# Optimization experiments

Measured on AMD Instinct MI355X. Metric: run time of the kernel, lower is better.

Reference implementation:

```python
import jax, jax.numpy as jnp
import numpy as np

GROUPS = 8
EPS = 1e-5


def setup_inputs() -> dict:
    key = jax.random.key(0)
    ks = jax.random.split(key, 4)
    B, C, H, W = 8, 128, 128, 128
    s = 1.0 / np.sqrt(C)
    return {
        "x": jax.random.normal(ks[0], (B, C, H, W), dtype=jnp.float32),
        "Wq": jax.random.normal(ks[1], (C, C), dtype=jnp.float32) * s,
        "bq": jnp.zeros((C,), jnp.float32),
        "Wk": jax.random.normal(ks[2], (C, C), dtype=jnp.float32) * s,
        "bk": jnp.zeros((C,), jnp.float32),
        "Wv": jax.random.normal(ks[3], (C, C), dtype=jnp.float32) * s,
        "bv": jnp.zeros((C,), jnp.float32),
        "gn_weight": jnp.ones((C,), jnp.float32),
        "gn_bias": jnp.zeros((C,), jnp.float32),
    }


def _group_norm(x_bcs, weight, bias):
    # x_bcs: [B, C, S]; GroupNorm over (C//G, S) per group
    B, C, S = x_bcs.shape
    xg = x_bcs.reshape(B, GROUPS, C // GROUPS, S)
    mean = xg.mean(axis=(2, 3), keepdims=True)
    var = jnp.mean(jnp.square(xg - mean), axis=(2, 3), keepdims=True)
    xn = ((xg - mean) * jax.lax.rsqrt(var + EPS)).reshape(B, C, S)
    return xn * weight[None, :, None] + bias[None, :, None]


def reference(x, Wq, bq, Wk, bk, Wv, bv, gn_weight, gn_bias):
    B, C, H, W = x.shape
    xs = x.reshape(B, C, H * W).transpose(0, 2, 1)  # [B, S, C]
    Q = xs @ Wq.T + bq
    K = xs @ Wk.T + bk
    V = xs @ Wv.T + bv
    Q = jax.nn.softmax(Q, axis=1)  # softmax over seq dim
    K = jax.nn.softmax(K, axis=1)
    KV = jnp.einsum('bsc,bsd->bcd', K, V)   # [B, C, C]
    Z = jnp.einsum('bsc,bcd->bsd', Q, KV)   # [B, S, C]
    xs = xs + Z
    x_gn = _group_norm(xs.transpose(0, 2, 1), gn_weight, gn_bias)  # [B, C, S]
    # Faithful to original: permute to [B, S, C] then view as [B, C, H, W]
    out = x_gn.transpose(0, 2, 1).reshape(B, C, H, W)
    return out
```

## Files before the change

kernel.cpp:

```cpp
#include <hip/hip_runtime.h>


#define Bn 8
#define Cn 128
#define Sn 16384
#define Gn 8

typedef float f32x4 __attribute__((ext_vector_type(4)));
typedef __bf16 bf16x8 __attribute__((ext_vector_type(8)));
typedef __bf16 bf16x4 __attribute__((ext_vector_type(4)));
typedef unsigned short u16;

__device__ __forceinline__ u16 f2bf(float f) {
    __bf16 h = (__bf16)f;
    return __builtin_bit_cast(u16, h);
}

__global__ __launch_bounds__(256) void k_wconv(const float* __restrict__ Wq,
                                               const float* __restrict__ Wk,
                                               const float* __restrict__ Wv,
                                               u16* __restrict__ Wb) {
    int i = blockIdx.x * 256 + threadIdx.x;
    const float* src = (i < 16384) ? Wq : (i < 32768 ? Wk : Wv);
    int j = i & 16383;
    Wb[i] = f2bf(src[j]);
}

__global__ __launch_bounds__(256) void k_tr(const float* __restrict__ x, u16* __restrict__ XT) {
    __shared__ float t[64][65];
    const int b = blockIdx.z, c0 = blockIdx.y * 64, s0 = blockIdx.x * 64;
    const int tid = threadIdx.x;
    const float* xb = x + ((size_t)b * Cn + c0) * Sn + s0;
#pragma unroll
    for (int i = 0; i < 16; ++i) {
        int n = tid + i * 256;
        int cl = n >> 6, sl = n & 63;
        t[cl][sl] = xb[(size_t)cl * Sn + sl];
    }
    __syncthreads();
    u16* xtb = XT + ((size_t)b * Sn + s0) * Cn + c0;
#pragma unroll
    for (int i = 0; i < 16; ++i) {
        int n = tid + i * 256;
        int sl = n >> 6, cl = n & 63;
        xtb[(size_t)sl * Cn + cl] = f2bf(t[cl][sl]);
    }
}

__device__ __forceinline__ bf16x8 lds_frag128(const u16* lds, int row, int c_off) {
    int ch = c_off >> 3;
    return *(const bf16x8*)(&lds[row * Cn + ((ch ^ (row & 7)) << 3)]);
}

__global__ __launch_bounds__(256) void k_qkv(
    const u16* __restrict__ XT, const u16* __restrict__ Wb,
    const float* __restrict__ bq, const float* __restrict__ bk, const float* __restrict__ bv,
    u16* __restrict__ EQ, u16* __restrict__ EK, u16* __restrict__ Vt,
    float* __restrict__ Zq, float* __restrict__ Zk) {
    __shared__ __align__(16) u16 tile[128 * 128];
    const int b = blockIdx.y;
    const int s0 = blockIdx.x * 128;
    const int tid = threadIdx.x;
    const int w = tid >> 6, l = tid & 63;
    const int l15 = l & 15, lq = l >> 4;

    {
        const u16* g = XT + ((size_t)b * Sn + s0) * Cn;
#pragma unroll
        for (int i = 0; i < 8; ++i) {
            int n = tid + i * 256, row = n >> 4, ch = n & 15;
            bf16x8 v = *(const bf16x8*)(g + row * Cn + ch * 8);
            *(bf16x8*)(&tile[row * Cn + ((ch ^ (row & 7)) << 3)]) = v;
        }
    }
    __syncthreads();

    const u16* Wqb = Wb;
    const u16* Wkb = Wb + 16384;
    const u16* Wvb = Wb + 32768;

    {
        bf16x8 a[2][4];
#pragma unroll
        for (int m = 0; m < 2; ++m)
#pragma unroll
            for (int k = 0; k < 4; ++k) {
                int row = 32 * w + 16 * m + l15;
                a[m][k] = *(const bf16x8*)(Wqb + row * Cn + 32 * k + lq * 8);
            }
        f32x4 acc[2][8];
#pragma unroll
        for (int m = 0; m < 2; ++m)
#pragma unroll
            for (int n = 0; n < 8; ++n)
#pragma unroll
                for (int r = 0; r < 4; ++r) acc[m][n][r] = 0.f;
#pragma unroll
        for (int n = 0; n < 8; ++n)
#pragma unroll
            for (int k = 0; k < 4; ++k) {
                bf16x8 bf = lds_frag128(tile, 16 * n + l15, 32 * k + lq * 8);
                acc[0][n] = __builtin_amdgcn_mfma_f32_16x16x32_bf16(a[0][k], bf, acc[0][n], 0, 0, 0);
                acc[1][n] = __builtin_amdgcn_mfma_f32_16x16x32_bf16(a[1][k], bf, acc[1][n], 0, 0, 0);
            }
        float zq[2][4] = {};
        float bqv[2][4];
#pragma unroll
        for (int m = 0; m < 2; ++m)
#pragma unroll
            for (int r = 0; r < 4; ++r) bqv[m][r] = bq[32 * w + 16 * m + lq * 4 + r];
#pragma unroll
        for (int m = 0; m < 2; ++m) {
            int cp = 32 * w + 16 * m + lq * 4;
#pragma unroll
            for (int n = 0; n < 8; ++n) {
                int s = s0 + 16 * n + l15;
                bf16x4 pk;
#pragma unroll
                for (int r = 0; r < 4; ++r) {
                    float e = __expf(acc[m][n][r] + bqv[m][r]);
                    zq[m][r] += e;
                    pk[r] = (__bf16)e;
                }
                *(bf16x4*)(&EQ[((size_t)b * Sn + s) * Cn + cp]) = pk;
            }
        }
#pragma unroll
        for (int m = 0; m < 2; ++m)
#pragma unroll
            for (int r = 0; r < 4; ++r) {
                float v = zq[m][r];
                v += __shfl_xor(v, 1);
                v += __shfl_xor(v, 2);
                v += __shfl_xor(v, 4);
                v += __shfl_xor(v, 8);
                if (l15 == 0) atomicAdd(&Zq[b * Cn + 32 * w + 16 * m + lq * 4 + r], v);
            }
    }

    bf16x8 am[2][4];
#pragma unroll
    for (int m = 0; m < 2; ++m)
#pragma unroll
        for (int k = 0; k < 4; ++k)
            am[m][k] = lds_frag128(tile, 32 * w + 16 * m + l15, 32 * k + lq * 8);

#pragma unroll
    for (int pass = 0; pass < 2; ++pass) {
        const u16* Wp = pass ? Wvb : Wkb;
        const float* bp = pass ? bv : bk;
        u16* Op = pass ? Vt : EK;
        f32x4 acc[2][8];
#pragma unroll
        for (int m = 0; m < 2; ++m)
#pragma unroll
            for (int n = 0; n < 8; ++n)
#pragma unroll
                for (int r = 0; r < 4; ++r) acc[m][n][r] = 0.f;
        float bval[8];
#pragma unroll
        for (int n = 0; n < 8; ++n) bval[n] = bp[16 * n + l15];
#pragma unroll
        for (int n = 0; n < 8; ++n)
#pragma unroll
            for (int k = 0; k < 4; ++k) {
                bf16x8 bf = *(const bf16x8*)(Wp + (16 * n + l15) * Cn + 32 * k + lq * 8);
                acc[0][n] = __builtin_amdgcn_mfma_f32_16x16x32_bf16(am[0][k], bf, acc[0][n], 0, 0, 0);
                acc[1][n] = __builtin_amdgcn_mfma_f32_16x16x32_bf16(am[1][k], bf, acc[1][n], 0, 0, 0);
            }
        float zk[8] = {};
#pragma unroll
        for (int m = 0; m < 2; ++m) {
            int sb = s0 + 32 * w + 16 * m + lq * 4;
#pragma unroll
            for (int n = 0; n < 8; ++n) {
                int cp = 16 * n + l15;
                bf16x4 pk;
#pragma unroll
                for (int r = 0; r < 4; ++r) {
                    float e = acc[m][n][r] + bval[n];
                    if (pass == 0) {
                        e = __expf(e);
                        zk[n] += e;
                    }
                    pk[r] = (__bf16)e;
                }
                *(bf16x4*)(&Op[((size_t)b * Cn + cp) * Sn + sb]) = pk;
            }
        }
        if (pass == 0) {
#pragma unroll
            for (int n = 0; n < 8; ++n) {
                float v = zk[n];
                v += __shfl_xor(v, 16);
                v += __shfl_xor(v, 32);
                if (l < 16) atomicAdd(&Zk[b * Cn + 16 * n + l], v);
            }
        }
    }
}

__global__ __launch_bounds__(512) void k_kv(const u16* __restrict__ EK, const u16* __restrict__ Vt,
                                            float* __restrict__ KVu) {
    __shared__ __align__(16) u16 ekt[128 * 64];
    __shared__ __align__(16) u16 vtt[128 * 64];
    const int b = blockIdx.y, sw = blockIdx.x;
    const int tid = threadIdx.x, w = tid >> 6, l = tid & 63;
    const int l15 = l & 15, lq = l >> 4;
    f32x4 acc[8];
#pragma unroll
    for (int n = 0; n < 8; ++n)
#pragma unroll
        for (int r = 0; r < 4; ++r) acc[n][r] = 0.f;
    const u16* ekb = EK + (size_t)b * Cn * Sn;
    const u16* vtb = Vt + (size_t)b * Cn * Sn;
    for (int step = 0; step < 8; ++step) {
        int s0 = sw * 512 + step * 64;
        __syncthreads();
#pragma unroll
        for (int i = 0; i < 2; ++i) {
            int n = tid + i * 512, row = n >> 3, ch = n & 7;
            int lidx = row * 64 + ((ch ^ (row & 7)) << 3);
            *(bf16x8*)(&ekt[lidx]) = *(const bf16x8*)(ekb + (size_t)row * Sn + s0 + ch * 8);
            *(bf16x8*)(&vtt[lidx]) = *(const bf16x8*)(vtb + (size_t)row * Sn + s0 + ch * 8);
        }
        __syncthreads();
#pragma unroll
        for (int k = 0; k < 2; ++k) {
            int ach = 4 * k + lq;
            int arow = 16 * w + l15;
            bf16x8 af = *(const bf16x8*)(&ekt[arow * 64 + ((ach ^ (arow & 7)) << 3)]);
#pragma unroll
            for (int n = 0; n < 8; ++n) {
                int brow = 16 * n + l15;
                bf16x8 bf = *(const bf16x8*)(&vtt[brow * 64 + ((ach ^ (brow & 7)) << 3)]);
                acc[n] = __builtin_amdgcn_mfma_f32_16x16x32_bf16(af, bf, acc[n], 0, 0, 0);
            }
        }
    }
#pragma unroll
    for (int n = 0; n < 8; ++n)
#pragma unroll
        for (int r = 0; r < 4; ++r) {
            int c = 16 * w + lq * 4 + r, d = 16 * n + l15;
            atomicAdd(&KVu[((size_t)b * Cn + c) * Cn + d], acc[n][r]);
        }
}

__global__ __launch_bounds__(256) void k_kvnorm(const float* __restrict__ KVu,
                                                const float* __restrict__ Zq,
                                                const float* __restrict__ Zk,
                                                u16* __restrict__ KV2T) {
    __shared__ float zi[128];
    __shared__ u16 t[128 * 136];
    const int b = blockIdx.x, tid = threadIdx.x;
    if (tid < 128) zi[tid] = 1.f / (Zk[b * Cn + tid] * Zq[b * Cn + tid]);
    __syncthreads();
    for (int i = 0; i < 64; ++i) {
        int n = tid + i * 256, c = n >> 7, d = n & 127;
        t[c * 136 + d] = f2bf(KVu[((size_t)b * Cn + c) * Cn + d] * zi[c]);
    }
    __syncthreads();
    for (int i = 0; i < 64; ++i) {
        int n = tid + i * 256, d = n >> 7, c = n & 127;
        KV2T[((size_t)b * Cn + d) * Cn + c] = t[c * 136 + d];
    }
}

__global__ __launch_bounds__(256) void k_z(
    const u16* __restrict__ EQ, const u16* __restrict__ KV2T, const u16* __restrict__ XT,
    u16* __restrict__ ybuf, float* __restrict__ gsum, float* __restrict__ gsq) {
    __shared__ __align__(16) u16 tile[128 * 128];
    const int b = blockIdx.y, s0 = blockIdx.x * 128;
    const int tid = threadIdx.x, w = tid >> 6, l = tid & 63;
    const int l15 = l & 15, lq = l >> 4;
    {
        const u16* g = EQ + ((size_t)b * Sn + s0) * Cn;
#pragma unroll
        for (int i = 0; i < 8; ++i) {
            int n = tid + i * 256, row = n >> 4, ch = n & 15;
            bf16x8 v = *(const bf16x8*)(g + row * Cn + ch * 8);
            *(bf16x8*)(&tile[row * Cn + ((ch ^ (row & 7)) << 3)]) = v;
        }
    }
    __syncthreads();
    bf16x8 a[2][4];
#pragma unroll
    for (int m = 0; m < 2; ++m)
#pragma unroll
        for (int k = 0; k < 4; ++k) {
            int rd = 32 * w + 16 * m + l15;
            a[m][k] = *(const bf16x8*)(KV2T + ((size_t)b * Cn + rd) * Cn + 32 * k + lq * 8);
        }
    f32x4 acc[2][8];
#pragma unroll
    for (int m = 0; m < 2; ++m)
#pragma unroll
        for (int n = 0; n < 8; ++n)
#pragma unroll
            for (int r = 0; r < 4; ++r) acc[m][n][r] = 0.f;
#pragma unroll
    for (int n = 0; n < 8; ++n)
#pragma unroll
        for (int k = 0; k < 4; ++k) {
            bf16x8 bf = lds_frag128(tile, 16 * n + l15, 32 * k + lq * 8);
            acc[0][n] = __builtin_amdgcn_mfma_f32_16x16x32_bf16(a[0][k], bf, acc[0][n], 0, 0, 0);
            acc[1][n] = __builtin_amdgcn_mfma_f32_16x16x32_bf16(a[1][k], bf, acc[1][n], 0, 0, 0);
        }
    float sm[2] = {0.f, 0.f}, sq[2] = {0.f, 0.f};
#pragma unroll
    for (int m = 0; m < 2; ++m) {
        int db = 32 * w + 16 * m + lq * 4;
#pragma unroll
        for (int n = 0; n < 8; ++n) {
            int s = s0 + 16 * n + l15;
            bf16x4 xv = *(const bf16x4*)(XT + ((size_t)b * Sn + s) * Cn + db);
            bf16x4 yk;
#pragma unroll
            for (int r = 0; r < 4; ++r) {
                float yv = (float)xv[r] + acc[m][n][r];
                sm[m] += yv;
                sq[m] += yv * yv;
                yk[r] = (__bf16)yv;
            }
            *(bf16x4*)(&ybuf[((size_t)b * Sn + s) * Cn + db]) = yk;
        }
    }
#pragma unroll
    for (int m = 0; m < 2; ++m) {
        float v1 = sm[m], v2 = sq[m];
#pragma unroll
        for (int mask = 1; mask < 64; mask <<= 1) {
            v1 += __shfl_xor(v1, mask);
            v2 += __shfl_xor(v2, mask);
        }
        if (l == 0) {
            int g = 2 * w + m;
            atomicAdd(&gsum[b * Gn + g], v1);
            atomicAdd(&gsq[b * Gn + g], v2);
        }
    }
}

__global__ __launch_bounds__(256) void k_gn(const u16* __restrict__ ybuf,
                                            const float* __restrict__ gsum,
                                            const float* __restrict__ gsq,
                                            const float* __restrict__ gnw,
                                            const float* __restrict__ gnb,
                                            float* __restrict__ out) {
    const float invN = 1.f / (float)(16 * Sn);
    size_t idx = (size_t)blockIdx.x * 256 + threadIdx.x;
    const size_t total = (size_t)Bn * Sn * Cn / 8;
    for (; idx < total; idx += (size_t)gridDim.x * 256) {
        size_t e0 = idx * 8;
        int c0 = (int)(e0 & 127);
        int b = (int)(e0 >> 21);
        int g = c0 >> 4;
        float mean = gsum[b * Gn + g] * invN;
        float var = gsq[b * Gn + g] * invN - mean * mean;
        float rstd = rsqrtf(var + 1e-5f);
        bf16x8 yv = *(const bf16x8*)(ybuf + e0);
        f32x4 o0, o1;
#pragma unroll
        for (int r = 0; r < 4; ++r) o0[r] = ((float)yv[r] - mean) * rstd * gnw[c0 + r] + gnb[c0 + r];
#pragma unroll
        for (int r = 0; r < 4; ++r) o1[r] = ((float)yv[4 + r] - mean) * rstd * gnw[c0 + 4 + r] + gnb[c0 + 4 + r];
        *(f32x4*)(out + e0) = o0;
        *(f32x4*)(out + e0 + 4) = o1;
    }
}

static constexpr size_t XT_OFF = 0;
static constexpr size_t EQ_OFF = 33554432;
static constexpr size_t EK_OFF = 67108864;
static constexpr size_t VT_OFF = 100663296;
static constexpr size_t WB_OFF = 134217728;
static constexpr size_t KVU_OFF = WB_OFF + 98304;
static constexpr size_t ZQ_OFF = KVU_OFF + 524288;
static constexpr size_t ZK_OFF = ZQ_OFF + 4096;
static constexpr size_t GSUM_OFF = ZK_OFF + 4096;
static constexpr size_t GSQ_OFF = GSUM_OFF + 256;
static constexpr size_t KV2T_OFF = GSQ_OFF + 256;
static constexpr size_t MEMSET_BYTES = 524288 + 4096 + 4096 + 256 + 256;

extern "C" void kernel_launch(void* const* d_in, const int* in_sizes, int n_in,
                              void* d_out, int out_size, void* d_ws, size_t ws_size,
                              hipStream_t stream) {
    const float* x = (const float*)d_in[0];
    const float* Wq = (const float*)d_in[1];
    const float* bq = (const float*)d_in[2];
    const float* Wk = (const float*)d_in[3];
    const float* bk = (const float*)d_in[4];
    const float* Wv = (const float*)d_in[5];
    const float* bv = (const float*)d_in[6];
    const float* gnw = (const float*)d_in[7];
    const float* gnb = (const float*)d_in[8];
    float* out = (float*)d_out;
    char* ws = (char*)d_ws;

    u16* XT = (u16*)(ws + XT_OFF);
    u16* EQ = (u16*)(ws + EQ_OFF);
    u16* EK = (u16*)(ws + EK_OFF);
    u16* Vt = (u16*)(ws + VT_OFF);
    u16* Wb = (u16*)(ws + WB_OFF);
    float* KVu = (float*)(ws + KVU_OFF);
    float* Zq = (float*)(ws + ZQ_OFF);
    float* Zk = (float*)(ws + ZK_OFF);
    float* Gsum = (float*)(ws + GSUM_OFF);
    float* Gsq = (float*)(ws + GSQ_OFF);
    u16* KV2T = (u16*)(ws + KV2T_OFF);
    u16* Ybuf = EK;

    hipMemsetAsync(ws + KVU_OFF, 0, MEMSET_BYTES, stream);
    k_wconv<<<dim3(192), dim3(256), 0, stream>>>(Wq, Wk, Wv, Wb);
    k_tr<<<dim3(Sn / 64, Cn / 64, Bn), dim3(256), 0, stream>>>(x, XT);
    k_qkv<<<dim3(Sn / 128, Bn), dim3(256), 0, stream>>>(XT, Wb, bq, bk, bv, EQ, EK, Vt, Zq, Zk);
    k_kv<<<dim3(32, Bn), dim3(512), 0, stream>>>(EK, Vt, KVu);
    k_kvnorm<<<dim3(Bn), dim3(256), 0, stream>>>(KVu, Zq, Zk, KV2T);
    k_z<<<dim3(Sn / 128, Bn), dim3(256), 0, stream>>>(EQ, KV2T, XT, Ybuf, Gsum, Gsq);
    k_gn<<<dim3(8192), dim3(256), 0, stream>>>(Ybuf, Gsum, Gsq, gnw, gnb, out);
}
```

Baseline: 338.5 us.

## Halve seq tiles in qkv/z kernels, vectorize transpose, reduce Zk atomics via LDS

The transpose kernel now uses float4 global loads and 16-byte bf16x8 stores in place of scalar accesses. k_qkv and k_z process 64-row sequence tiles instead of 128, which doubles the grid and cuts LDS and register use per block. k_qkv also reduces the Zk partial sums across waves in shared memory before issuing one atomic per channel. k_kv uses fewer blocks, each covering a longer sequence range. Together these aim for better occupancy and memory efficiency, at the cost of reloading the weight fragments in more blocks and issuing more Zq atomics.

```diff
diff --git a/kernel.cpp b/kernel.cpp
--- a/kernel.cpp
+++ b/kernel.cpp
@@ -32,18 +32,23 @@
     const int tid = threadIdx.x;
     const float* xb = x + ((size_t)b * Cn + c0) * Sn + s0;
 #pragma unroll
-    for (int i = 0; i < 16; ++i) {
+    for (int i = 0; i < 4; ++i) {
         int n = tid + i * 256;
-        int cl = n >> 6, sl = n & 63;
-        t[cl][sl] = xb[(size_t)cl * Sn + sl];
+        int cl = n >> 4, s4 = (n & 15) * 4;
+        f32x4 v = *(const f32x4*)(xb + (size_t)cl * Sn + s4);
+#pragma unroll
+        for (int j = 0; j < 4; ++j) t[cl][s4 + j] = v[j];
     }
     __syncthreads();
     u16* xtb = XT + ((size_t)b * Sn + s0) * Cn + c0;
 #pragma unroll
-    for (int i = 0; i < 16; ++i) {
+    for (int i = 0; i < 2; ++i) {
         int n = tid + i * 256;
-        int sl = n >> 6, cl = n & 63;
-        xtb[(size_t)sl * Cn + cl] = f2bf(t[cl][sl]);
+        int sl = n >> 3, cl0 = (n & 7) * 8;
+        bf16x8 o;
+#pragma unroll
+        for (int j = 0; j < 8; ++j) o[j] = (__bf16)t[cl0 + j][sl];
+        *(bf16x8*)(xtb + sl * Cn + cl0) = o;
     }
 }
 
@@ -57,9 +62,10 @@
     const float* __restrict__ bq, const float* __restrict__ bk, const float* __restrict__ bv,
     u16* __restrict__ EQ, u16* __restrict__ EK, u16* __restrict__ Vt,
     float* __restrict__ Zq, float* __restrict__ Zk) {
-    __shared__ __align__(16) u16 tile[128 * 128];
+    __shared__ __align__(16) u16 tile[64 * 128];
+    __shared__ float zbuf[4 * 128];
     const int b = blockIdx.y;
-    const int s0 = blockIdx.x * 128;
+    const int s0 = blockIdx.x * 64;
     const int tid = threadIdx.x;
     const int w = tid >> 6, l = tid & 63;
     const int l15 = l & 15, lq = l >> 4;
@@ -67,7 +73,7 @@
     {
         const u16* g = XT + ((size_t)b * Sn + s0) * Cn;
 #pragma unroll
-        for (int i = 0; i < 8; ++i) {
+        for (int i = 0; i < 4; ++i) {
             int n = tid + i * 256, row = n >> 4, ch = n & 15;
             bf16x8 v = *(const bf16x8*)(g + row * Cn + ch * 8);
             *(bf16x8*)(&tile[row * Cn + ((ch ^ (row & 7)) << 3)]) = v;
@@ -88,15 +94,15 @@
                 int row = 32 * w + 16 * m + l15;
                 a[m][k] = *(const bf16x8*)(Wqb + row * Cn + 32 * k + lq * 8);
             }
-        f32x4 acc[2][8];
+        f32x4 acc[2][4];
 #pragma unroll
         for (int m = 0; m < 2; ++m)
 #pragma unroll
-            for (int n = 0; n < 8; ++n)
+            for (int n = 0; n < 4; ++n)
 #pragma unroll
                 for (int r = 0; r < 4; ++r) acc[m][n][r] = 0.f;
 #pragma unroll
-        for (int n = 0; n < 8; ++n)
+        for (int n = 0; n < 4; ++n)
 #pragma unroll
             for (int k = 0; k < 4; ++k) {
                 bf16x8 bf = lds_frag128(tile, 16 * n + l15, 32 * k + lq * 8);
@@ -113,7 +119,7 @@
         for (int m = 0; m < 2; ++m) {
             int cp = 32 * w + 16 * m + lq * 4;
 #pragma unroll
-            for (int n = 0; n < 8; ++n) {
+            for (int n = 0; n < 4; ++n) {
                 int s = s0 + 16 * n + l15;
                 bf16x4 pk;
 #pragma unroll
@@ -138,25 +144,21 @@
             }
     }
 
-    bf16x8 am[2][4];
-#pragma unroll
-    for (int m = 0; m < 2; ++m)
-#pragma unroll
-        for (int k = 0; k < 4; ++k)
-            am[m][k] = lds_frag128(tile, 32 * w + 16 * m + l15, 32 * k + lq * 8);
+    bf16x8 am[4];
+#pragma unroll
+    for (int k = 0; k < 4; ++k)
+        am[k] = lds_frag128(tile, 16 * w + l15, 32 * k + lq * 8);
 
 #pragma unroll
     for (int pass = 0; pass < 2; ++pass) {
         const u16* Wp = pass ? Wvb : Wkb;
         const float* bp = pass ? bv : bk;
         u16* Op = pass ? Vt : EK;
-        f32x4 acc[2][8];
-#pragma unroll
-        for (int m = 0; m < 2; ++m)
-#pragma unroll
-            for (int n = 0; n < 8; ++n)
-#pragma unroll
-                for (int r = 0; r < 4; ++r) acc[m][n][r] = 0.f;
+        f32x4 acc[8];
+#pragma unroll
+        for (int n = 0; n < 8; ++n)
+#pragma unroll
+            for (int r = 0; r < 4; ++r) acc[n][r] = 0.f;
         float bval[8];
 #pragma unroll
         for (int n = 0; n < 8; ++n) bval[n] = bp[16 * n + l15];
@@ -165,28 +167,24 @@
 #pragma unroll
             for (int k = 0; k < 4; ++k) {
                 bf16x8 bf = *(const bf16x8*)(Wp + (16 * n + l15) * Cn + 32 * k + lq * 8);
-                acc[0][n] = __builtin_amdgcn_mfma_f32_16x16x32_bf16(am[0][k], bf, acc[0][n], 0, 0, 0);
-                acc[1][n] = __builtin_amdgcn_mfma_f32_16x16x32_bf16(am[1][k], bf, acc[1][n], 0, 0, 0);
+                acc[n] = __builtin_amdgcn_mfma_f32_16x16x32_bf16(am[k], bf, acc[n], 0, 0, 0);
             }
         float zk[8] = {};
-#pragma unroll
-        for (int m = 0; m < 2; ++m) {
-            int sb = s0 + 32 * w + 16 * m + lq * 4;
-#pragma unroll
-            for (int n = 0; n < 8; ++n) {
-                int cp = 16 * n + l15;
-                bf16x4 pk;
-#pragma unroll
-                for (int r = 0; r < 4; ++r) {
-                    float e = acc[m][n][r] + bval[n];
-                    if (pass == 0) {
-                        e = __expf(e);
-                        zk[n] += e;
-                    }
-                    pk[r] = (__bf16)e;
+        int sb = s0 + 16 * w + lq * 4;
+#pragma unroll
+        for (int n = 0; n < 8; ++n) {
+            int cp = 16 * n + l15;
+            bf16x4 pk;
+#pragma unroll
+            for (int r = 0; r < 4; ++r) {
+                float e = acc[n][r] + bval[n];
+                if (pass == 0) {
+                    e = __expf(e);
+                    zk[n] += e;
                 }
-                *(bf16x4*)(&Op[((size_t)b * Cn + cp) * Sn + sb]) = pk;
-            }
+                pk[r] = (__bf16)e;
+            }
+            *(bf16x4*)(&Op[((size_t)b * Cn + cp) * Sn + sb]) = pk;
         }
         if (pass == 0) {
 #pragma unroll
@@ -194,9 +192,14 @@
                 float v = zk[n];
                 v += __shfl_xor(v, 16);
                 v += __shfl_xor(v, 32);
-                if (l < 16) atomicAdd(&Zk[b * Cn + 16 * n + l], v);
-            }
-        }
+                if (l < 16) zbuf[w * 128 + 16 * n + l] = v;
+            }
+        }
+    }
+    __syncthreads();
+    if (tid < 128) {
+        float v = zbuf[tid] + zbuf[128 + tid] + zbuf[256 + tid] + zbuf[384 + tid];
+        atomicAdd(&Zk[b * Cn + tid], v);
     }
 }
 
@@ -214,8 +217,8 @@
         for (int r = 0; r < 4; ++r) acc[n][r] = 0.f;
     const u16* ekb = EK + (size_t)b * Cn * Sn;
     const u16* vtb = Vt + (size_t)b * Cn * Sn;
-    for (int step = 0; step < 8; ++step) {
-        int s0 = sw * 512 + step * 64;
+    for (int step = 0; step < 16; ++step) {
+        int s0 = sw * 1024 + step * 64;
         __syncthreads();
 #pragma unroll
         for (int i = 0; i < 2; ++i) {
@@ -270,14 +273,14 @@
 __global__ __launch_bounds__(256) void k_z(
     const u16* __restrict__ EQ, const u16* __restrict__ KV2T, const u16* __restrict__ XT,
     u16* __restrict__ ybuf, float* __restrict__ gsum, float* __restrict__ gsq) {
-    __shared__ __align__(16) u16 tile[128 * 128];
-    const int b = blockIdx.y, s0 = blockIdx.x * 128;
+    __shared__ __align__(16) u16 tile[64 * 128];
+    const int b = blockIdx.y, s0 = blockIdx.x * 64;
     const int tid = threadIdx.x, w = tid >> 6, l = tid & 63;
     const int l15 = l & 15, lq = l >> 4;
     {
         const u16* g = EQ + ((size_t)b * Sn + s0) * Cn;
 #pragma unroll
-        for (int i = 0; i < 8; ++i) {
+        for (int i = 0; i < 4; ++i) {
             int n = tid + i * 256, row = n >> 4, ch = n & 15;
             bf16x8 v = *(const bf16x8*)(g + row * Cn + ch * 8);
             *(bf16x8*)(&tile[row * Cn + ((ch ^ (row & 7)) << 3)]) = v;
@@ -292,15 +295,15 @@
             int rd = 32 * w + 16 * m + l15;
             a[m][k] = *(const bf16x8*)(KV2T + ((size_t)b * Cn + rd) * Cn + 32 * k + lq * 8);
         }
-    f32x4 acc[2][8];
+    f32x4 acc[2][4];
 #pragma unroll
     for (int m = 0; m < 2; ++m)
 #pragma unroll
-        for (int n = 0; n < 8; ++n)
+        for (int n = 0; n < 4; ++n)
 #pragma unroll
             for (int r = 0; r < 4; ++r) acc[m][n][r] = 0.f;
 #pragma unroll
-    for (int n = 0; n < 8; ++n)
+    for (int n = 0; n < 4; ++n)
 #pragma unroll
         for (int k = 0; k < 4; ++k) {
             bf16x8 bf = lds_frag128(tile, 16 * n + l15, 32 * k + lq * 8);
@@ -312,7 +315,7 @@
     for (int m = 0; m < 2; ++m) {
         int db = 32 * w + 16 * m + lq * 4;
 #pragma unroll
-        for (int n = 0; n < 8; ++n) {
+        for (int n = 0; n < 4; ++n) {
             int s = s0 + 16 * n + l15;
             bf16x4 xv = *(const bf16x4*)(XT + ((size_t)b * Sn + s) * Cn + db);
             bf16x4 yk;
@@ -414,9 +417,9 @@
     hipMemsetAsync(ws + KVU_OFF, 0, MEMSET_BYTES, stream);
     k_wconv<<<dim3(192), dim3(256), 0, stream>>>(Wq, Wk, Wv, Wb);
     k_tr<<<dim3(Sn / 64, Cn / 64, Bn), dim3(256), 0, stream>>>(x, XT);
-    k_qkv<<<dim3(Sn / 128, Bn), dim3(256), 0, stream>>>(XT, Wb, bq, bk, bv, EQ, EK, Vt, Zq, Zk);
-    k_kv<<<dim3(32, Bn), dim3(512), 0, stream>>>(EK, Vt, KVu);
+    k_qkv<<<dim3(Sn / 64, Bn), dim3(256), 0, stream>>>(XT, Wb, bq, bk, bv, EQ, EK, Vt, Zq, Zk);
+    k_kv<<<dim3(16, Bn), dim3(512), 0, stream>>>(EK, Vt, KVu);
     k_kvnorm<<<dim3(Bn), dim3(256), 0, stream>>>(KVu, Zq, Zk, KV2T);
-    k_z<<<dim3(Sn / 128, Bn), dim3(256), 0, stream>>>(EQ, KV2T, XT, Ybuf, Gsum, Gsq);
+    k_z<<<dim3(Sn / 64, Bn), dim3(256), 0, stream>>>(EQ, KV2T, XT, Ybuf, Gsum, Gsq);
     k_gn<<<dim3(8192), dim3(256), 0, stream>>>(Ybuf, Gsum, Gsq, gnw, gnb, out);
 }
```

New measurement: 465.2 us. 1.37x slower.

## Stage kernel outputs through LDS for coalesced stores and vectorize transpose

Applied to the files above, without the earlier changes.

The transpose kernel now uses 16-byte float4 loads and 8-wide bf16 stores. The QKV kernel stages its EQ, EK and Vt outputs through swizzled shared memory so each is written as full coalesced rows, and it reduces the Zk partial sums per block before issuing atomics. The Z kernel processes two 128-row tiles per block, reads the residual XT through LDS, and writes ybuf through LDS with coalesced stores, which halves the grid and the number of atomics. These changes target scattered 8-byte global stores and strided loads, at the cost of extra barriers and LDS traffic.

```diff
diff --git a/kernel.cpp b/kernel.cpp
--- a/kernel.cpp
+++ b/kernel.cpp
@@ -32,24 +32,38 @@
     const int tid = threadIdx.x;
     const float* xb = x + ((size_t)b * Cn + c0) * Sn + s0;
 #pragma unroll
-    for (int i = 0; i < 16; ++i) {
+    for (int i = 0; i < 4; ++i) {
         int n = tid + i * 256;
-        int cl = n >> 6, sl = n & 63;
-        t[cl][sl] = xb[(size_t)cl * Sn + sl];
+        int cl = n >> 4, s4 = (n & 15) * 4;
+        f32x4 v = *(const f32x4*)(xb + (size_t)cl * Sn + s4);
+#pragma unroll
+        for (int j = 0; j < 4; ++j) t[cl][s4 + j] = v[j];
     }
     __syncthreads();
     u16* xtb = XT + ((size_t)b * Sn + s0) * Cn + c0;
 #pragma unroll
-    for (int i = 0; i < 16; ++i) {
+    for (int i = 0; i < 2; ++i) {
         int n = tid + i * 256;
-        int sl = n >> 6, cl = n & 63;
-        xtb[(size_t)sl * Cn + cl] = f2bf(t[cl][sl]);
+        int sl = n >> 3, cl0 = (n & 7) * 8;
+        bf16x8 o;
+#pragma unroll
+        for (int j = 0; j < 8; ++j) o[j] = (__bf16)t[cl0 + j][sl];
+        *(bf16x8*)(xtb + sl * Cn + cl0) = o;
     }
 }
 
 __device__ __forceinline__ bf16x8 lds_frag128(const u16* lds, int row, int c_off) {
     int ch = c_off >> 3;
     return *(const bf16x8*)(&lds[row * Cn + ((ch ^ (row & 7)) << 3)]);
+}
+__device__ __forceinline__ int lds_addr8(int row, int col) {
+    return row * Cn + ((((col >> 3) ^ (row & 7))) << 3) + (col & 7);
+}
+__device__ __forceinline__ void lds_write8(u16* lds, int row, int col, bf16x4 v) {
+    *(bf16x4*)(&lds[lds_addr8(row, col)]) = v;
+}
+__device__ __forceinline__ bf16x4 lds_read8(const u16* lds, int row, int col) {
+    return *(const bf16x4*)(&lds[lds_addr8(row, col)]);
 }
 
 __global__ __launch_bounds__(256) void k_qkv(
@@ -58,6 +72,7 @@
     u16* __restrict__ EQ, u16* __restrict__ EK, u16* __restrict__ Vt,
     float* __restrict__ Zq, float* __restrict__ Zk) {
     __shared__ __align__(16) u16 tile[128 * 128];
+    __shared__ float zbuf[4 * 128];
     const int b = blockIdx.y;
     const int s0 = blockIdx.x * 128;
     const int tid = threadIdx.x;
@@ -79,6 +94,13 @@
     const u16* Wkb = Wb + 16384;
     const u16* Wvb = Wb + 32768;
 
+    bf16x8 am[2][4];
+#pragma unroll
+    for (int m = 0; m < 2; ++m)
+#pragma unroll
+        for (int k = 0; k < 4; ++k)
+            am[m][k] = lds_frag128(tile, 32 * w + 16 * m + l15, 32 * k + lq * 8);
+
     {
         bf16x8 a[2][4];
 #pragma unroll
@@ -109,22 +131,17 @@
         for (int m = 0; m < 2; ++m)
 #pragma unroll
             for (int r = 0; r < 4; ++r) bqv[m][r] = bq[32 * w + 16 * m + lq * 4 + r];
-#pragma unroll
-        for (int m = 0; m < 2; ++m) {
-            int cp = 32 * w + 16 * m + lq * 4;
-#pragma unroll
-            for (int n = 0; n < 8; ++n) {
-                int s = s0 + 16 * n + l15;
-                bf16x4 pk;
+        bf16x4 pkq[2][8];
+#pragma unroll
+        for (int m = 0; m < 2; ++m)
+#pragma unroll
+            for (int n = 0; n < 8; ++n)
 #pragma unroll
                 for (int r = 0; r < 4; ++r) {
                     float e = __expf(acc[m][n][r] + bqv[m][r]);
                     zq[m][r] += e;
-                    pk[r] = (__bf16)e;
+                    pkq[m][n][r] = (__bf16)e;
                 }
-                *(bf16x4*)(&EQ[((size_t)b * Sn + s) * Cn + cp]) = pk;
-            }
-        }
 #pragma unroll
         for (int m = 0; m < 2; ++m)
 #pragma unroll
@@ -136,14 +153,24 @@
                 v += __shfl_xor(v, 8);
                 if (l15 == 0) atomicAdd(&Zq[b * Cn + 32 * w + 16 * m + lq * 4 + r], v);
             }
-    }
-
-    bf16x8 am[2][4];
-#pragma unroll
-    for (int m = 0; m < 2; ++m)
-#pragma unroll
-        for (int k = 0; k < 4; ++k)
-            am[m][k] = lds_frag128(tile, 32 * w + 16 * m + l15, 32 * k + lq * 8);
+        __syncthreads();
+#pragma unroll
+        for (int m = 0; m < 2; ++m) {
+            int cp = 32 * w + 16 * m + lq * 4;
+#pragma unroll
+            for (int n = 0; n < 8; ++n) lds_write8(tile, 16 * n + l15, cp, pkq[m][n]);
+        }
+        __syncthreads();
+        {
+            u16* g = EQ + ((size_t)b * Sn + s0) * Cn;
+#pragma unroll
+            for (int i = 0; i < 8; ++i) {
+                int n = tid + i * 256, row = n >> 4, ch = n & 15;
+                bf16x8 v = *(const bf16x8*)(&tile[row * Cn + ((ch ^ (row & 7)) << 3)]);
+                *(bf16x8*)(g + row * Cn + ch * 8) = v;
+            }
+        }
+    }
 
 #pragma unroll
     for (int pass = 0; pass < 2; ++pass) {
@@ -169,13 +196,11 @@
                 acc[1][n] = __builtin_amdgcn_mfma_f32_16x16x32_bf16(am[1][k], bf, acc[1][n], 0, 0, 0);
             }
         float zk[8] = {};
-#pragma unroll
-        for (int m = 0; m < 2; ++m) {
-            int sb = s0 + 32 * w + 16 * m + lq * 4;
-#pragma unroll
-            for (int n = 0; n < 8; ++n) {
-                int cp = 16 * n + l15;
-                bf16x4 pk;
+        bf16x4 pk[2][8];
+#pragma unroll
+        for (int m = 0; m < 2; ++m)
+#pragma unroll
+            for (int n = 0; n < 8; ++n)
 #pragma unroll
                 for (int r = 0; r < 4; ++r) {
                     float e = acc[m][n][r] + bval[n];
@@ -183,20 +208,36 @@
                         e = __expf(e);
                         zk[n] += e;
                     }
-                    pk[r] = (__bf16)e;
+                    pk[m][n][r] = (__bf16)e;
                 }
-                *(bf16x4*)(&Op[((size_t)b * Cn + cp) * Sn + sb]) = pk;
-            }
-        }
         if (pass == 0) {
 #pragma unroll
             for (int n = 0; n < 8; ++n) {
                 float v = zk[n];
                 v += __shfl_xor(v, 16);
                 v += __shfl_xor(v, 32);
-                if (l < 16) atomicAdd(&Zk[b * Cn + 16 * n + l], v);
-            }
-        }
+                if (l < 16) zbuf[w * 128 + 16 * n + l] = v;
+            }
+        }
+        __syncthreads();
+#pragma unroll
+        for (int m = 0; m < 2; ++m) {
+            int sl = 32 * w + 16 * m + lq * 4;
+#pragma unroll
+            for (int n = 0; n < 8; ++n) lds_write8(tile, 16 * n + l15, sl, pk[m][n]);
+        }
+        __syncthreads();
+#pragma unroll
+        for (int i = 0; i < 8; ++i) {
+            int n = tid + i * 256, row = n >> 4, ch = n & 15;
+            bf16x8 v = *(const bf16x8*)(&tile[row * Cn + ((ch ^ (row & 7)) << 3)]);
+            *(bf16x8*)(&Op[((size_t)b * Cn + row) * Sn + s0 + ch * 8]) = v;
+        }
+    }
+    __syncthreads();
+    if (tid < 128) {
+        float v = zbuf[tid] + zbuf[128 + tid] + zbuf[256 + tid] + zbuf[384 + tid];
+        atomicAdd(&Zk[b * Cn + tid], v);
     }
 }
 
@@ -271,19 +312,10 @@
     const u16* __restrict__ EQ, const u16* __restrict__ KV2T, const u16* __restrict__ XT,
     u16* __restrict__ ybuf, float* __restrict__ gsum, float* __restrict__ gsq) {
     __shared__ __align__(16) u16 tile[128 * 128];
-    const int b = blockIdx.y, s0 = blockIdx.x * 128;
+    const int b = blockIdx.y;
     const int tid = threadIdx.x, w = tid >> 6, l = tid & 63;
     const int l15 = l & 15, lq = l >> 4;
-    {
-        const u16* g = EQ + ((size_t)b * Sn + s0) * Cn;
-#pragma unroll
-        for (int i = 0; i < 8; ++i) {
-            int n = tid + i * 256, row = n >> 4, ch = n & 15;
-            bf16x8 v = *(const bf16x8*)(g + row * Cn + ch * 8);
-            *(bf16x8*)(&tile[row * Cn + ((ch ^ (row & 7)) << 3)]) = v;
-        }
-    }
-    __syncthreads();
+
     bf16x8 a[2][4];
 #pragma unroll
     for (int m = 0; m < 2; ++m)
@@ -292,40 +324,78 @@
             int rd = 32 * w + 16 * m + l15;
             a[m][k] = *(const bf16x8*)(KV2T + ((size_t)b * Cn + rd) * Cn + 32 * k + lq * 8);
         }
-    f32x4 acc[2][8];
-#pragma unroll
-    for (int m = 0; m < 2; ++m)
+
+    float sm[2] = {0.f, 0.f}, sq[2] = {0.f, 0.f};
+
+    for (int t = 0; t < 2; ++t) {
+        const int s0 = (blockIdx.x * 2 + t) * 128;
+        if (t) __syncthreads();
+        {
+            const u16* g = EQ + ((size_t)b * Sn + s0) * Cn;
+#pragma unroll
+            for (int i = 0; i < 8; ++i) {
+                int n = tid + i * 256, row = n >> 4, ch = n & 15;
+                bf16x8 v = *(const bf16x8*)(g + row * Cn + ch * 8);
+                *(bf16x8*)(&tile[row * Cn + ((ch ^ (row & 7)) << 3)]) = v;
+            }
+        }
+        __syncthreads();
+        f32x4 acc[2][8];
+#pragma unroll
+        for (int m = 0; m < 2; ++m)
+#pragma unroll
+            for (int n = 0; n < 8; ++n)
+#pragma unroll
+                for (int r = 0; r < 4; ++r) acc[m][n][r] = 0.f;
 #pragma unroll
         for (int n = 0; n < 8; ++n)
 #pragma unroll
-            for (int r = 0; r < 4; ++r) acc[m][n][r] = 0.f;
-#pragma unroll
-    for (int n = 0; n < 8; ++n)
-#pragma unroll
-        for (int k = 0; k < 4; ++k) {
-            bf16x8 bf = lds_frag128(tile, 16 * n + l15, 32 * k + lq * 8);
-            acc[0][n] = __builtin_amdgcn_mfma_f32_16x16x32_bf16(a[0][k], bf, acc[0][n], 0, 0, 0);
-            acc[1][n] = __builtin_amdgcn_mfma_f32_16x16x32_bf16(a[1][k], bf, acc[1][n], 0, 0, 0);
-        }
-    float sm[2] = {0.f, 0.f}, sq[2] = {0.f, 0.f};
-#pragma unroll
-    for (int m = 0; m < 2; ++m) {
-        int db = 32 * w + 16 * m + lq * 4;
-#pragma unroll
-        for (int n = 0; n < 8; ++n) {
-            int s = s0 + 16 * n + l15;
-            bf16x4 xv = *(const bf16x4*)(XT + ((size_t)b * Sn + s) * Cn + db);
-            bf16x4 yk;
-#pragma unroll
-            for (int r = 0; r < 4; ++r) {
-                float yv = (float)xv[r] + acc[m][n][r];
-                sm[m] += yv;
-                sq[m] += yv * yv;
-                yk[r] = (__bf16)yv;
-            }
-            *(bf16x4*)(&ybuf[((size_t)b * Sn + s) * Cn + db]) = yk;
-        }
-    }
+            for (int k = 0; k < 4; ++k) {
+                bf16x8 bf = lds_frag128(tile, 16 * n + l15, 32 * k + lq * 8);
+                acc[0][n] = __builtin_amdgcn_mfma_f32_16x16x32_bf16(a[0][k], bf, acc[0][n], 0, 0, 0);
+                acc[1][n] = __builtin_amdgcn_mfma_f32_16x16x32_bf16(a[1][k], bf, acc[1][n], 0, 0, 0);
+            }
+        __syncthreads();
+        {
+            const u16* g = XT + ((size_t)b * Sn + s0) * Cn;
+#pragma unroll
+            for (int i = 0; i < 8; ++i) {
+                int n = tid + i * 256, row = n >> 4, ch = n & 15;
+                bf16x8 v = *(const bf16x8*)(g + row * Cn + ch * 8);
+                *(bf16x8*)(&tile[row * Cn + ((ch ^ (row & 7)) << 3)]) = v;
+            }
+        }
+        __syncthreads();
+#pragma unroll
+        for (int m = 0; m < 2; ++m) {
+            int db = 32 * w + 16 * m + lq * 4;
+#pragma unroll
+            for (int n = 0; n < 8; ++n) {
+                int row = 16 * n + l15;
+                bf16x4 xv = lds_read8(tile, row, db);
+                bf16x4 yk;
+#pragma unroll
+                for (int r = 0; r < 4; ++r) {
+                    float yv = (float)xv[r] + acc[m][n][r];
+                    sm[m] += yv;
+                    sq[m] += yv * yv;
+                    yk[r] = (__bf16)yv;
+                }
+                lds_write8(tile, row, db, yk);
+            }
+        }
+        __syncthreads();
+        {
+            u16* g = ybuf + ((size_t)b * Sn + s0) * Cn;
+#pragma unroll
+            for (int i = 0; i < 8; ++i) {
+                int n = tid + i * 256, row = n >> 4, ch = n & 15;
+                bf16x8 v = *(const bf16x8*)(&tile[row * Cn + ((ch ^ (row & 7)) << 3)]);
+                *(bf16x8*)(g + row * Cn + ch * 8) = v;
+            }
+        }
+    }
+
 #pragma unroll
     for (int m = 0; m < 2; ++m) {
         float v1 = sm[m], v2 = sq[m];
@@ -417,6 +487,6 @@
     k_qkv<<<dim3(Sn / 128, Bn), dim3(256), 0, stream>>>(XT, Wb, bq, bk, bv, EQ, EK, Vt, Zq, Zk);
     k_kv<<<dim3(32, Bn), dim3(512), 0, stream>>>(EK, Vt, KVu);
     k_kvnorm<<<dim3(Bn), dim3(256), 0, stream>>>(KVu, Zq, Zk, KV2T);
-    k_z<<<dim3(Sn / 128, Bn), dim3(256), 0, stream>>>(EQ, KV2T, XT, Ybuf, Gsum, Gsq);
+    k_z<<<dim3(Sn / 256, Bn), dim3(256), 0, stream>>>(EQ, KV2T, XT, Ybuf, Gsum, Gsq);
     k_gn<<<dim3(8192), dim3(256), 0, stream>>>(Ybuf, Gsum, Gsq, gnw, gnb, out);
 }
```

New measurement: 287.0 us. 15.2% less time.
